# Kernel optimization log

Hardware: AMD Instinct MI355X
Metric: run time of the kernel (lower is better)

## Reference

```python
import jax, jax.numpy as jnp
import numpy as np

BETA = 0.1  # 0.1 + 0.1*sin(t/1000) at t=0

def setup_inputs() -> dict:
    key = jax.random.key(0)
    k1, k2 = jax.random.split(key)
    x_cat = jax.random.uniform(k1, (256, 64, 64), dtype=jnp.float32, minval=1e-6, maxval=1.0)
    u = jax.random.uniform(k2, (256, 64, 64), dtype=jnp.float32, minval=1e-6, maxval=1.0 - 1e-6)
    noise = -jnp.log(-jnp.log(u))  # standard Gumbel(0,1)
    return {"x_cat": x_cat, "noise": noise}

def reference(x_cat, noise):
    B, A, k = x_cat.shape
    P = A // 2
    x = x_cat.reshape(B, P, 2, k)          # [B,P,2,k]: axis 0 = horiz, 1 = vert
    h, v = x[:, :, 0], x[:, :, 1]
    # outer product per (batch, place): [B,P,k] x [B,P,k] -> [B,P,k,k]
    places = jnp.einsum('bpj,bpk->bpjk', h, v)
    # Gumbel-argmax sampling: pdf * 1[log(pdf)+beta*g == max over k]
    log_pdf = jnp.log(x) + BETA * noise.reshape(B, P, 2, k)
    mx = jnp.max(log_pdf, axis=-1, keepdims=True)
    sampled = x * (log_pdf == mx).astype(x.dtype)
    sampled_points = jnp.einsum('bpj,bpk->bpjk', sampled[:, :, 0], sampled[:, :, 1]) * 100.0
    return (places, sampled_points)
```

## Files before the change

### kernel.cpp

```cpp
#include <hip/hip_runtime.h>
#include <math.h>


#define BETA 0.1f
#define PLACES_ELEMS 33554432ull

typedef float vfloat4 __attribute__((ext_vector_type(4)));

__global__ __launch_bounds__(256) void fused_sampler(
    const float* __restrict__ x_cat,
    const float* __restrict__ noise,
    float* __restrict__ out)
{
    const int b   = blockIdx.x;
    const int tid = threadIdx.x;

    if (b < 8192) {
        const int bp = b;
        const float* __restrict__ xrow = x_cat + (size_t)bp * 128;
        vfloat4* __restrict__ pout = (vfloat4*)out + (size_t)bp * 1024;

        const int c  = tid & 15;
        const int j0 = tid >> 4;
        const vfloat4 v4 = *(const vfloat4*)(xrow + 64 + 4 * c);

        #pragma unroll
        for (int it = 0; it < 4; ++it) {
            const int j = j0 + 16 * it;
            const float hj = xrow[j];
            pout[j * 16 + c] = hj * v4;
        }
    } else {
        const int bp   = b - 8192;
        const int lane = tid & 63;
        const float* __restrict__ xrow = x_cat + (size_t)bp * 128;
        const float* __restrict__ nrow = noise + (size_t)bp * 128;

        const float h = xrow[lane];
        const float v = xrow[64 + lane];
        float lph = logf(h) + BETA * nrow[lane];
        float lpv = logf(v) + BETA * nrow[64 + lane];
        int   jh  = lane;
        int   jv  = lane;

        #pragma unroll
        for (int off = 32; off > 0; off >>= 1) {
            const float oh = __shfl_xor(lph, off, 64);
            const int   oi = __shfl_xor(jh,  off, 64);
            const float ov = __shfl_xor(lpv, off, 64);
            const int   oj = __shfl_xor(jv,  off, 64);
            if (oh > lph || (oh == lph && oi < jh)) { lph = oh; jh = oi; }
            if (ov > lpv || (ov == lpv && oj < jv)) { lpv = ov; jv = oj; }
        }
        const float sval = 100.0f * __shfl(h, jh, 64) * __shfl(v, jv, 64);

        vfloat4* __restrict__ sout =
            (vfloat4*)(out + PLACES_ELEMS) + (size_t)bp * 1024;
        const int kjv = jv >> 2;
        const int mjv = jv & 3;

        const int c  = tid & 15;
        const int j0 = tid >> 4;

        #pragma unroll
        for (int it = 0; it < 4; ++it) {
            const int j = j0 + 16 * it;
            const bool hit = (j == jh) & (c == kjv);
            vfloat4 sv;
            sv.x = (hit && mjv == 0) ? sval : 0.f;
            sv.y = (hit && mjv == 1) ? sval : 0.f;
            sv.z = (hit && mjv == 2) ? sval : 0.f;
            sv.w = (hit && mjv == 3) ? sval : 0.f;
            sout[j * 16 + c] = sv;
        }
    }
}

extern "C" void kernel_launch(void* const* d_in, const int* in_sizes, int n_in,
                              void* d_out, int out_size, void* d_ws, size_t ws_size,
                              hipStream_t stream) {
    const float* x_cat = (const float*)d_in[0];
    const float* noise = (const float*)d_in[1];
    float* out = (float*)d_out;

    fused_sampler<<<dim3(16384), dim3(256), 0, stream>>>(x_cat, noise, out);
}
```

Measured before the change: 271.6 us.

## Assign one wavefront per place instead of one block per place

Each 64-lane wavefront now handles a whole (batch, place) pair, writing 16 float4 stores per lane, and the grid shrinks from 16384 to 4096 blocks. The aim is to cut block launch and scheduling overhead and to amortise index math, and in the sampling path it also avoids the four waves of a block each redoing the same reduction. The cost is more stores in flight per thread and fewer threads overall to hide write latency. The kernel is write-bound on a 256MB output.

```diff
diff --git a/kernel.cpp b/kernel.cpp
--- a/kernel.cpp
+++ b/kernel.cpp
@@ -12,27 +12,26 @@
     const float* __restrict__ noise,
     float* __restrict__ out)
 {
-    const int b   = blockIdx.x;
-    const int tid = threadIdx.x;
+    const int w    = blockIdx.x * 4 + (threadIdx.x >> 6);
+    const int lane = threadIdx.x & 63;
+    const int c    = lane & 15;
+    const int j0   = lane >> 4;
 
-    if (b < 8192) {
-        const int bp = b;
+    if (w < 8192) {
+        const int bp = w;
         const float* __restrict__ xrow = x_cat + (size_t)bp * 128;
         vfloat4* __restrict__ pout = (vfloat4*)out + (size_t)bp * 1024;
 
-        const int c  = tid & 15;
-        const int j0 = tid >> 4;
         const vfloat4 v4 = *(const vfloat4*)(xrow + 64 + 4 * c);
+        float h[16];
+        #pragma unroll
+        for (int r = 0; r < 16; ++r) h[r] = xrow[j0 + 4 * r];
 
         #pragma unroll
-        for (int it = 0; it < 4; ++it) {
-            const int j = j0 + 16 * it;
-            const float hj = xrow[j];
-            pout[j * 16 + c] = hj * v4;
-        }
+        for (int r = 0; r < 16; ++r)
+            pout[lane + 64 * r] = h[r] * v4;
     } else {
-        const int bp   = b - 8192;
-        const int lane = tid & 63;
+        const int bp = w - 8192;
         const float* __restrict__ xrow = x_cat + (size_t)bp * 128;
         const float* __restrict__ nrow = noise + (size_t)bp * 128;
 
@@ -59,19 +58,16 @@
         const int kjv = jv >> 2;
         const int mjv = jv & 3;
 
-        const int c  = tid & 15;
-        const int j0 = tid >> 4;
-
         #pragma unroll
-        for (int it = 0; it < 4; ++it) {
-            const int j = j0 + 16 * it;
+        for (int r = 0; r < 16; ++r) {
+            const int j = j0 + 4 * r;
             const bool hit = (j == jh) & (c == kjv);
             vfloat4 sv;
             sv.x = (hit && mjv == 0) ? sval : 0.f;
             sv.y = (hit && mjv == 1) ? sval : 0.f;
             sv.z = (hit && mjv == 2) ? sval : 0.f;
             sv.w = (hit && mjv == 3) ? sval : 0.f;
-            sout[j * 16 + c] = sv;
+            sout[lane + 64 * r] = sv;
         }
     }
 }
@@ -83,5 +79,5 @@
     const float* noise = (const float*)d_in[1];
     float* out = (float*)d_out;
 
-    fused_sampler<<<dim3(16384), dim3(256), 0, stream>>>(x_cat, noise, out);
+    fused_sampler<<<dim3(4096), dim3(256), 0, stream>>>(x_cat, noise, out);
 }
```

Measured after the change: 267.4 us. Within noise of the previous version (-1.6%).
